# Kernel optimization log

Hardware: AMD Instinct MI355X
Metric: run time of the kernel (lower is better)

Reference implementation:

```python
import jax, jax.numpy as jnp
import numpy as np

N = 96        # num_nodes
D = 64        # emb_size / n_hid
BS = 16
T = 13
G = 1         # num_graph

# all N^2 ordered pairs, receiver-major: edge e=i*N+j has receiver i, sender j
_REC = jnp.repeat(jnp.arange(N), N)
_SEND = jnp.tile(jnp.arange(N), N)


def _lin(shape, key, scale=0.05):
    return (jax.random.normal(key, shape, dtype=jnp.float32) * scale)


def setup_inputs() -> dict:
    key = jax.random.key(0)
    ks = jax.random.split(key, 24)
    inp = {
        "skill_seq": jax.random.randint(ks[0], (BS, T), 0, N, dtype=jnp.int32),
        "adj": jax.random.uniform(ks[1], (G, BS, N, N), dtype=jnp.float32),
        "node_embeddings": jax.random.normal(ks[2], (G, N, D), dtype=jnp.float32),
        # edge MLP
        "W_msg1": _lin((2 * D, D), ks[3]), "b_msg1": jnp.zeros((D,), jnp.float32),
        "W_msg2": _lin((D, D), ks[4]),     "b_msg2": jnp.zeros((D,), jnp.float32),
        # GRU hidden projections (no bias)
        "W_hr": _lin((D, D), ks[5]), "W_hi": _lin((D, D), ks[6]), "W_hh": _lin((D, D), ks[7]),
        # GRU input projections (bias)
        "W_ir": _lin((D, D), ks[8]),  "b_ir": jnp.zeros((D,), jnp.float32),
        "W_ii": _lin((D, D), ks[9]),  "b_ii": jnp.zeros((D,), jnp.float32),
        "W_in": _lin((D, D), ks[10]), "b_in": jnp.zeros((D,), jnp.float32),
        # output MLP
        "W_o1": _lin((D, D), ks[11]), "b_o1": jnp.zeros((D,), jnp.float32),
        "W_o2": _lin((D, D), ks[12]), "b_o2": jnp.zeros((D,), jnp.float32),
        "W_o3": _lin((D, D), ks[13]), "b_o3": jnp.zeros((D,), jnp.float32),
    }
    return inp


def _forward(skill_seq, adj, node_embeddings,
             W_msg1, b_msg1, W_msg2, b_msg2,
             W_hr, W_hi, W_hh,
             W_ir, b_ir, W_ii, b_ii, W_in, b_in,
             W_o1, b_o1, W_o2, b_o2, W_o3, b_o3):
    bs, time_steps = skill_seq.shape
    hidden0 = jnp.zeros((G, bs, N, D), dtype=adj.dtype)
    emb = node_embeddings[0]  # [N, D] (num_graph=1)

    def step(hidden, skill_t):
        # gather senders/receivers over the node axis -> [G, bs, N^2, 2D]
        senders = hidden[:, :, _SEND, :]
        receivers = hidden[:, :, _REC, :]
        pre_msg = jnp.concatenate([senders, receivers], axis=-1)
        msg = jnp.tanh(pre_msg @ W_msg1 + b_msg1)        # [G, bs, N^2, D]
        msg = jnp.tanh(msg @ W_msg2 + b_msg2)
        msg = msg.reshape(G, bs, N, N, D)                # receiver i, sender j
        # mask by adjacency and scatter-sum over senders, then /N
        agg = jnp.einsum('gbij,gbijd->gbid', adj, msg) / N   # [G, bs, N, D]
        inputs = emb[skill_t][None, :, None, :]          # [1, bs, 1, D]
        r = jax.nn.sigmoid(inputs @ W_ir + b_ir + agg @ W_hr)
        i = jax.nn.sigmoid(inputs @ W_ii + b_ii + agg @ W_hi)
        n = jnp.tanh(inputs @ W_in + b_in + r * (agg @ W_hh))
        hidden = (1.0 - i) * n + i * hidden
        pred = jax.nn.relu(hidden @ W_o1 + b_o1)
        pred = jax.nn.relu(pred @ W_o2 + b_o2)
        pred = pred @ W_o3 + b_o3                        # [G, bs, N, D]
        return hidden, pred

    skills_t = skill_seq[:, :time_steps - 1].T           # [T-1, bs]
    _, preds = jax.lax.scan(step, hidden0, skills_t)     # [T-1, G, bs, N, D]
    # torch: stack(dim=1) -> [G, T-1, bs, N, D]; transpose(1,2) -> [G, bs, T-1, N, D]
    return jnp.transpose(preds, (1, 2, 0, 3, 4))


def reference(skill_seq, adj, node_embeddings,
              W_msg1, b_msg1, W_msg2, b_msg2,
              W_hr, W_hi, W_hh,
              W_ir, b_ir, W_ii, b_ii, W_in, b_in,
              W_o1, b_o1, W_o2, b_o2, W_o3, b_o3):
    return _forward(skill_seq, adj, node_embeddings,
                    W_msg1, b_msg1, W_msg2, b_msg2,
                    W_hr, W_hi, W_hh,
                    W_ir, b_ir, W_ii, b_ii, W_in, b_in,
                    W_o1, b_o1, W_o2, b_o2, W_o3, b_o3)
```

## Files before the change

### kernel.cpp

```cpp
#include <hip/hip_runtime.h>

typedef unsigned short ushort_t;
typedef __attribute__((ext_vector_type(8))) short short8;
typedef __attribute__((ext_vector_type(8))) __bf16 bf16x8;
typedef __attribute__((ext_vector_type(4))) float floatx4;

#define NN 96
#define DD 64
#define BSZ 16
#define TSTEP 12
#define JSPLIT 4
#define JPW 24
#define ITILES 6

#define OFF_HALL  0u
#define OFF_E     5111808u
#define OFF_S0    5185536u
#define OFF_S1    5578752u
#define OFF_R0    5971968u
#define OFF_R1    6365184u
#define OFF_PART  6758400u
#define OFF_WSWZ  9904128u
#define OFF_CNT   9977856u
#define HSLOT     98304

union fragU  { short8 s; bf16x8 b; };
union packU  { floatx4 f; unsigned long long u[2]; };

static __device__ __forceinline__ short f2bf(float f){
    union { float f; unsigned u; } v; v.f = f;
    unsigned u = v.u;
    u += 0x7fffu + ((u >> 16) & 1u);
    return (short)(u >> 16);
}
static __device__ __forceinline__ float fast_tanh(float x){
    float p = __expf(2.f * x);
    return (p - 1.f) * __builtin_amdgcn_rcpf(p + 1.f);
}
static __device__ __forceinline__ float fast_sigmoid(float x){
    float p = __expf(-x);
    return __builtin_amdgcn_rcpf(1.f + p);
}
static __device__ __forceinline__ void zero4(floatx4* a){
    floatx4 z = {0.f,0.f,0.f,0.f};
    a[0]=z; a[1]=z; a[2]=z; a[3]=z;
}
static __device__ __forceinline__ floatx4 aload4(const float* p){
    const unsigned long long* s = (const unsigned long long*)p;
    packU pk;
    pk.u[0] = __hip_atomic_load(s,     __ATOMIC_RELAXED, __HIP_MEMORY_SCOPE_AGENT);
    pk.u[1] = __hip_atomic_load(s + 1, __ATOMIC_RELAXED, __HIP_MEMORY_SCOPE_AGENT);
    return pk.f;
}
static __device__ __forceinline__ void astore4(float* p, floatx4 v){
    unsigned long long* d = (unsigned long long*)p;
    packU pk; pk.f = v;
    __hip_atomic_store(d,     pk.u[0], __ATOMIC_RELAXED, __HIP_MEMORY_SCOPE_AGENT);
    __hip_atomic_store(d + 1, pk.u[1], __ATOMIC_RELAXED, __HIP_MEMORY_SCOPE_AGENT);
}
static __device__ __forceinline__ void buildA(const float* sM, int col, int quad, short8& a0, short8& a1){
    floatx4 f0 = *(const floatx4*)&sM[col*68 + quad*8];
    floatx4 f1 = *(const floatx4*)&sM[col*68 + quad*8 + 4];
    floatx4 f2 = *(const floatx4*)&sM[col*68 + 32 + quad*8];
    floatx4 f3 = *(const floatx4*)&sM[col*68 + 32 + quad*8 + 4];
    fragU u0, u1;
    #pragma unroll
    for (int jj = 0; jj < 4; jj++){
        u0.b[jj]   = (__bf16)f0[jj];
        u0.b[4+jj] = (__bf16)f1[jj];
        u1.b[jj]   = (__bf16)f2[jj];
        u1.b[4+jj] = (__bf16)f3[jj];
    }
    a0 = u0.s; a1 = u1.s;
}
static __device__ __forceinline__ void mm16(short8 a0, short8 a1, const short8* wzm, int l, floatx4* acc){
    #pragma unroll
    for (int nt = 0; nt < 4; nt++){
        short8 b0 = wzm[nt*64 + l];
        short8 b1 = wzm[(4 + nt)*64 + l];
        acc[nt] = __builtin_amdgcn_mfma_f32_16x16x32_bf16(a0, b0, acc[nt], 0, 0, 0);
        acc[nt] = __builtin_amdgcn_mfma_f32_16x16x32_bf16(a1, b1, acc[nt], 0, 0, 0);
    }
}
static __device__ __forceinline__ void mm16r(short8 a0, short8 a1, const short8* f, floatx4* acc){
    #pragma unroll
    for (int nt = 0; nt < 4; nt++){
        acc[nt] = __builtin_amdgcn_mfma_f32_16x16x32_bf16(a0, f[nt],     acc[nt], 0, 0, 0);
        acc[nt] = __builtin_amdgcn_mfma_f32_16x16x32_bf16(a1, f[4 + nt], acc[nt], 0, 0, 0);
    }
}

__global__ __launch_bounds__(256) void k_init(
    const float* __restrict__ emb, const float* __restrict__ Wmsg1,
    const float* __restrict__ Wmsg2,
    const float* __restrict__ Whr, const float* __restrict__ Whi, const float* __restrict__ Whh,
    const float* __restrict__ Wir, const float* __restrict__ bir,
    const float* __restrict__ Wii, const float* __restrict__ bii,
    const float* __restrict__ Win, const float* __restrict__ bin,
    const float* __restrict__ Wo1, const float* __restrict__ Wo2, const float* __restrict__ Wo3,
    int* __restrict__ cnt, float* __restrict__ Ef, ushort_t* __restrict__ wswz)
{
    int wg = blockIdx.x, tid = threadIdx.x;
    if (wg < 72) {
        int flat = wg*256 + tid;
        int m = flat / 6144; int r = flat % 6144; int s = r >> 6; int d = r & 63;
        const float* W = (m==0)? Wir : (m==1)? Wii : Win;
        const float* B = (m==0)? bir : (m==1)? bii : bin;
        float acc = B[d];
        #pragma unroll 8
        for (int k = 0; k < 64; k++)
            acc += emb[s*64 + k] * W[k*64 + d];
        Ef[flat] = acc;
        if (wg < 5) {
            int c = wg*256 + tid;
            if (c < TSTEP*BSZ*ITILES) cnt[c] = 0;
        }
    } else {
        int flat = (wg - 72)*256 + tid;
        int m = flat >> 12; int q = flat & 4095;
        int jj = q & 7, lane = (q >> 3) & 63, nt = (q >> 9) & 3, kc = q >> 11;
        int k = kc*32 + ((lane >> 4) << 3) + jj;
        int n = nt*16 + (lane & 15);
        const float* src; int idx = k*64 + n;
        switch (m) {
          case 0: src = Wmsg2; break;
          case 1: src = Whr;  break;
          case 2: src = Whi;  break;
          case 3: src = Whh;  break;
          case 4: src = Wmsg1; break;
          case 5: src = Wmsg1; idx = (64 + k)*64 + n; break;
          case 6: src = Wo1; break;
          case 7: src = Wo2; break;
          default: src = Wo3; break;
        }
        wswz[flat] = (ushort_t)f2bf(src[idx]);
    }
}

__global__ __launch_bounds__(256) void k_step0(
    const float* __restrict__ adj, const float* __restrict__ b1in, const float* __restrict__ b2in,
    const int* __restrict__ skills, const float* __restrict__ Ef,
    const ushort_t* __restrict__ wswz,
    float* __restrict__ hall, float* __restrict__ S1, float* __restrict__ R1)
{
    __shared__ float sM[16*68];
    __shared__ float sG[3][16*68];
    __shared__ float sE[3*64];
    __shared__ float sRS[16*17];
    int wg = blockIdx.x; int b = wg / 6, it = wg % 6;
    int tid = threadIdx.x; int w = tid >> 6; int l = tid & 63;
    int quad = l >> 4, col = l & 15;

    {
        int i = tid >> 4, seg = tid & 15;
        const float* arow = &adj[(b*NN + it*16 + i)*NN + seg*6];
        float s = 0.f;
        #pragma unroll
        for (int j = 0; j < 6; j++) s += arow[j];
        sRS[i*17 + seg] = s;
    }
    if (tid < 192) {
        int s = skills[b*13 + 0];
        sE[tid] = Ef[(tid >> 6)*6144 + s*64 + (tid & 63)];
    }
    __syncthreads();
    if (tid < 16) {
        float s = 0.f;
        #pragma unroll
        for (int q = 0; q < 16; q++) s += sRS[tid*17 + q];
        sRS[tid*17 + 16] = s * (1.f/96.f);
    }
    __syncthreads();

    if (w == 0) {
        float b2v[4];
        #pragma unroll
        for (int nt = 0; nt < 4; nt++) b2v[nt] = b2in[nt*16 + col];
        fragU u0, u1;
        #pragma unroll
        for (int e = 0; e < 8; e++) {
            u0.b[e] = (__bf16)fast_tanh(b1in[quad*8 + e]);
            u1.b[e] = (__bf16)fast_tanh(b1in[32 + quad*8 + e]);
        }
        floatx4 acc[4];
        zero4(acc);
        mm16(u0.s, u1.s, (const short8*)wswz + 0*512, l, acc);
        #pragma unroll
        for (int nt = 0; nt < 4; nt++)
          #pragma unroll
          for (int r = 0; r < 4; r++) {
            float m = fast_tanh(acc[nt][r] + b2v[nt]);
            sM[(quad*4 + r)*68 + nt*16 + col] = sRS[(quad*4 + r)*17 + 16] * m;
          }
    }
    __syncthreads();

    if (w < 3) {
        short8 a0, a1;
        buildA(sM, col, quad, a0, a1);
        floatx4 acc[4];
        zero4(acc);
        mm16(a0, a1, (const short8*)wswz + (1 + w)*512, l, acc);
        #pragma unroll
        for (int nt = 0; nt < 4; nt++)
          #pragma unroll
          for (int r = 0; r < 4; r++)
            sG[w][(quad*4 + r)*68 + nt*16 + col] = acc[nt][r];
    }
    __syncthreads();

    {
        int i = tid >> 4, k4 = (tid & 15)*4;
        float h[4];
        #pragma unroll
        for (int e = 0; e < 4; e++) {
            int d = k4 + e;
            float gi = fast_sigmoid(sE[64 + d] + sG[1][i*68 + d]);
            float gr = fast_sigmoid(sE[d]      + sG[0][i*68 + d]);
            float nv = fast_tanh  (sE[128 + d] + gr * sG[2][i*68 + d]);
            h[e] = (1.f - gi)*nv;
        }
        #pragma unroll
        for (int e = 0; e < 4; e++) sM[i*68 + k4 + e] = h[e];
        floatx4 hv = { h[0], h[1], h[2], h[3] };
        *(floatx4*)&hall[(size_t)1*HSLOT + (b*NN + it*16 + i)*64 + k4] = hv;
    }
    __syncthreads();

    if (w < 2) {
        short8 a0, a1;
        buildA(sM, col, quad, a0, a1);
        floatx4 acc[4];
        zero4(acc);
        mm16(a0, a1, (const short8*)wswz + (4 + w)*512, l, acc);
        float* dst = (w == 0) ? S1 : R1;
        #pragma unroll
        for (int nt = 0; nt < 4; nt++)
          #pragma unroll
          for (int r = 0; r < 4; r++)
            dst[(b*NN + it*16 + quad*4 + r)*64 + nt*16 + col] = acc[nt][r];
    }
}

__global__ __launch_bounds__(512, 2) void k_step(
    const float* __restrict__ adj, const float* __restrict__ b1in, const float* __restrict__ b2in,
    const float* __restrict__ Sread, const float* __restrict__ Rread,
    const ushort_t* __restrict__ wswz, float* __restrict__ partial,
    const int* __restrict__ skills, const float* __restrict__ Ef,
    const float* __restrict__ hprev, float* __restrict__ hcur,
    float* __restrict__ Swrite, float* __restrict__ Rwrite,
    int* __restrict__ cnt, int t)
{
    __shared__ float lds[11712];
    __shared__ int sLast;
    float* sS   = lds;
    float* sRB  = lds + 1536;
    float* sAdj = lds + 2624;
    float* sAgg = lds + 3008;

    int wg = blockIdx.x;
    int js = wg / 96; int rem = wg % 96; int b = rem / 6; int it = rem % 6;
    int tid = threadIdx.x; int w = tid >> 6; int l = tid & 63;
    int quad = l >> 4, col = l & 15;
    int j0 = js * JPW;

    for (int q = tid; q < JPW*16; q += 512) {
        int row = q >> 4, c4 = (q & 15) * 4;
        *(floatx4*)&sS[row*64 + c4] = *(const floatx4*)&Sread[(b*NN + j0 + row)*64 + c4];
    }
    if (tid < 256) {
        int row = tid >> 4, c4 = (tid & 15) * 4;
        floatx4 r4 = *(const floatx4*)&Rread[(b*NN + it*16 + row)*64 + c4];
        floatx4 b4 = *(const floatx4*)&b1in[c4];
        floatx4 o = r4 + b4;
        *(floatx4*)&sRB[row*68 + c4] = o;
    }
    if (tid < 16*JPW) {
        int i = tid / JPW, j = tid % JPW;
        sAdj[tid] = adj[(b*NN + it*16 + i)*NN + j0 + j];
    }
    const short8* wz = (const short8*)wswz;
    short8 w2f[2][4];
    #pragma unroll
    for (int kc = 0; kc < 2; kc++)
      #pragma unroll
      for (int nt = 0; nt < 4; nt++)
        w2f[kc][nt] = wz[(kc*4 + nt)*64 + l];
    float b2v[4];
    #pragma unroll
    for (int nt = 0; nt < 4; nt++) b2v[nt] = b2in[nt*16 + col];
    __syncthreads();

    float rbv[16];
    #pragma unroll
    for (int c = 0; c < 4; c++)
        *(floatx4*)&rbv[c*4] = *(const floatx4*)&sRB[col*68 + (c>>1)*32 + quad*8 + (c&1)*4];

    float agg[4][4];
    #pragma unroll
    for (int nt=0;nt<4;nt++)
      #pragma unroll
      for (int r=0;r<4;r++) agg[nt][r] = 0.f;

    #pragma unroll
    for (int c = 0; c < 3; c++) {
        int jl = w*3 + c;
        float sv[16];
        #pragma unroll
        for (int cc = 0; cc < 4; cc++)
            *(floatx4*)&sv[cc*4] = *(const floatx4*)&sS[jl*64 + (cc>>1)*32 + quad*8 + (cc&1)*4];
        fragU u0, u1;
        #pragma unroll
        for (int e = 0; e < 8; e++) {
            u0.b[e] = (__bf16)fast_tanh(sv[e]   + rbv[e]);
            u1.b[e] = (__bf16)fast_tanh(sv[8+e] + rbv[8+e]);
        }
        floatx4 acc[4];
        zero4(acc);
        #pragma unroll
        for (int nt = 0; nt < 4; nt++) {
            acc[nt] = __builtin_amdgcn_mfma_f32_16x16x32_bf16(u0.s, w2f[0][nt], acc[nt], 0,0,0);
            acc[nt] = __builtin_amdgcn_mfma_f32_16x16x32_bf16(u1.s, w2f[1][nt], acc[nt], 0,0,0);
        }
        float adjv[4];
        #pragma unroll
        for (int r = 0; r < 4; r++) adjv[r] = sAdj[(quad*4 + r)*JPW + jl];
        #pragma unroll
        for (int nt = 0; nt < 4; nt++)
          #pragma unroll
          for (int r = 0; r < 4; r++)
            agg[nt][r] += adjv[r] * fast_tanh(acc[nt][r] + b2v[nt]);
    }
    #pragma unroll
    for (int nt = 0; nt < 4; nt++)
      #pragma unroll
      for (int r = 0; r < 4; r++)
        sAgg[w*1088 + (quad*4 + r)*68 + nt*16 + col] = agg[nt][r];
    __syncthreads();
    if (tid < 256) {
        int i = tid >> 4, k4 = (tid & 15) * 4;
        floatx4 o = {0.f,0.f,0.f,0.f};
        #pragma unroll
        for (int s8 = 0; s8 < 8; s8++)
            o += *(const floatx4*)&sAgg[s8*1088 + i*68 + k4];
        o = o * (1.f/96.f);
        astore4(&partial[((js*BSZ + b)*NN + it*16 + i)*64 + k4], o);
    }
    if (t == TSTEP - 1) return;

    __syncthreads();
    if (tid == 0) {
        int old = atomicAdd(&cnt[t*(BSZ*ITILES) + b*ITILES + it], 1);
        sLast = (old == JSPLIT - 1);
    }
    __syncthreads();
    if (!sLast) return;

    float* sM = lds;
    float* sG = lds + 1088;
    float* sH = lds + 4352;
    float* sE = lds + 5376;

    const short8* wzb = (const short8*)wswz;
    short8 fG[8], fSR[8];
    if (w < 3) {
        #pragma unroll
        for (int q = 0; q < 8; q++) fG[q] = wzb[(1 + w)*512 + q*64 + l];
    }
    if (w < 2) {
        #pragma unroll
        for (int q = 0; q < 8; q++) fSR[q] = wzb[(4 + w)*512 + q*64 + l];
    }

    if (tid < 256) {
        int i = tid >> 4, k4 = (tid & 15) * 4;
        floatx4 a = {0.f,0.f,0.f,0.f};
        #pragma unroll
        for (int p = 0; p < JSPLIT; p++)
            a += aload4(&partial[((p*BSZ + b)*NN + it*16 + i)*64 + k4]);
        *(floatx4*)&sM[i*68 + k4] = a;
        *(floatx4*)&sH[i*64 + k4] = *(const floatx4*)&hprev[(b*NN + it*16 + i)*64 + k4];
    } else if (tid < 448) {
        int q = tid - 256;
        int s = skills[b*13 + t];
        sE[q] = Ef[(q >> 6)*6144 + s*64 + (q & 63)];
    }
    __syncthreads();

    if (w < 3) {
        short8 a0, a1;
        buildA(sM, col, quad, a0, a1);
        floatx4 acc[4];
        zero4(acc);
        mm16r(a0, a1, fG, acc);
        #pragma unroll
        for (int nt = 0; nt < 4; nt++)
          #pragma unroll
          for (int r = 0; r < 4; r++)
            sG[w*1088 + (quad*4 + r)*68 + nt*16 + col] = acc[nt][r];
    }
    __syncthreads();

    if (tid < 256) {
        int i = tid >> 4, k4 = (tid & 15) * 4;
        float h[4];
        #pragma unroll
        for (int e = 0; e < 4; e++) {
            int d = k4 + e;
            float gr = fast_sigmoid(sE[d]       + sG[0*1088 + i*68 + d]);
            float gi = fast_sigmoid(sE[64 + d]  + sG[1*1088 + i*68 + d]);
            float nv = fast_tanh  (sE[128 + d] + gr * sG[2*1088 + i*68 + d]);
            h[e] = (1.f - gi)*nv + gi*sH[i*64 + d];
        }
        #pragma unroll
        for (int e = 0; e < 4; e++) sM[i*68 + k4 + e] = h[e];
        floatx4 hv = { h[0], h[1], h[2], h[3] };
        *(floatx4*)&hcur[(b*NN + it*16 + i)*64 + k4] = hv;
    }
    __syncthreads();

    if (w < 2) {
        short8 a0, a1;
        buildA(sM, col, quad, a0, a1);
        floatx4 acc[4];
        zero4(acc);
        mm16r(a0, a1, fSR, acc);
        float* dst = (w == 0) ? Swrite : Rwrite;
        #pragma unroll
        for (int nt = 0; nt < 4; nt++)
          #pragma unroll
          for (int r = 0; r < 4; r++)
            dst[(b*NN + it*16 + quad*4 + r)*64 + nt*16 + col] = acc[nt][r];
    }
}

__global__ __launch_bounds__(256) void k_out(
    const int* __restrict__ skills, const float* __restrict__ partial,
    const float* __restrict__ Ef, const float* __restrict__ hall,
    const ushort_t* __restrict__ wswz,
    const float* __restrict__ bo1, const float* __restrict__ bo2, const float* __restrict__ bo3,
    float* __restrict__ out)
{
    __shared__ float sT[4][16*68];
    int tid = threadIdx.x; int w = tid >> 6; int l = tid & 63;
    int quad = l >> 4, col = l & 15;
    int g = blockIdx.x*4 + w;
    int ts = g / 96; int rem = g % 96; int b = rem / 6, it = rem % 6;
    float* sm = sT[w];

    if (ts < 11) {
        const float* hsrc = hall + (size_t)(ts + 1)*HSLOT + (b*NN + it*16)*64;
        int i = l >> 2, c0 = (l & 3)*16;
        #pragma unroll
        for (int cc = 0; cc < 4; cc++)
            *(floatx4*)&sm[i*68 + c0 + cc*4] = *(const floatx4*)&hsrc[i*64 + c0 + cc*4];
    } else {
        int i = l >> 2, c0 = (l & 3)*16;
        floatx4 a[4]; zero4(a);
        for (int p = 0; p < JSPLIT; p++) {
            const float* base = &partial[((p*BSZ + b)*NN + it*16 + i)*64 + c0];
            #pragma unroll
            for (int cc = 0; cc < 4; cc++) a[cc] += *(const floatx4*)&base[cc*4];
        }
        #pragma unroll
        for (int cc = 0; cc < 4; cc++) *(floatx4*)&sm[i*68 + c0 + cc*4] = a[cc];

        short8 a0, a1; buildA(sm, col, quad, a0, a1);
        floatx4 Ar[4], Ai[4], Ah[4];
        zero4(Ar); zero4(Ai); zero4(Ah);
        mm16(a0, a1, (const short8*)wswz + 1*512, l, Ar);
        mm16(a0, a1, (const short8*)wswz + 2*512, l, Ai);
        mm16(a0, a1, (const short8*)wswz + 3*512, l, Ah);
        int s = skills[b*13 + 11];
        const float* hp = hall + 11*(size_t)HSLOT;
        #pragma unroll
        for (int nt = 0; nt < 4; nt++) {
            int d = nt*16 + col;
            float er = Ef[0*6144 + s*64 + d];
            float ei = Ef[1*6144 + s*64 + d];
            float en = Ef[2*6144 + s*64 + d];
            #pragma unroll
            for (int r = 0; r < 4; r++) {
                int row = it*16 + quad*4 + r;
                float gr = fast_sigmoid(er + Ar[nt][r]);
                float gi = fast_sigmoid(ei + Ai[nt][r]);
                float nv = fast_tanh  (en + gr*Ah[nt][r]);
                sm[(quad*4 + r)*68 + d] = (1.f - gi)*nv + gi*hp[(b*NN + row)*64 + d];
            }
        }
    }

    float bv1[4], bv2[4], bv3[4];
    #pragma unroll
    for (int nt = 0; nt < 4; nt++) {
        bv1[nt] = bo1[nt*16 + col];
        bv2[nt] = bo2[nt*16 + col];
        bv3[nt] = bo3[nt*16 + col];
    }
    short8 a0, a1;
    floatx4 acc[4];

    buildA(sm, col, quad, a0, a1);
    zero4(acc);
    mm16(a0, a1, (const short8*)wswz + 6*512, l, acc);
    #pragma unroll
    for (int nt = 0; nt < 4; nt++)
      #pragma unroll
      for (int r = 0; r < 4; r++)
        sm[(quad*4 + r)*68 + nt*16 + col] = fmaxf(0.f, acc[nt][r] + bv1[nt]);

    buildA(sm, col, quad, a0, a1);
    zero4(acc);
    mm16(a0, a1, (const short8*)wswz + 7*512, l, acc);
    #pragma unroll
    for (int nt = 0; nt < 4; nt++)
      #pragma unroll
      for (int r = 0; r < 4; r++)
        sm[(quad*4 + r)*68 + nt*16 + col] = fmaxf(0.f, acc[nt][r] + bv2[nt]);

    buildA(sm, col, quad, a0, a1);
    zero4(acc);
    mm16(a0, a1, (const short8*)wswz + 8*512, l, acc);
    #pragma unroll
    for (int nt = 0; nt < 4; nt++)
      #pragma unroll
      for (int r = 0; r < 4; r++)
        out[((b*TSTEP + ts)*NN + it*16 + quad*4 + r)*64 + nt*16 + col] = acc[nt][r] + bv3[nt];
}

extern "C" void kernel_launch(void* const* d_in, const int* in_sizes, int n_in,
                              void* d_out, int out_size, void* d_ws, size_t ws_size,
                              hipStream_t stream) {
    const int*   skills = (const int*)d_in[0];
    const float* adj    = (const float*)d_in[1];
    const float* emb    = (const float*)d_in[2];
    const float* Wmsg1  = (const float*)d_in[3];
    const float* b1     = (const float*)d_in[4];
    const float* Wmsg2  = (const float*)d_in[5];
    const float* b2     = (const float*)d_in[6];
    const float* Whr    = (const float*)d_in[7];
    const float* Whi    = (const float*)d_in[8];
    const float* Whh    = (const float*)d_in[9];
    const float* Wir    = (const float*)d_in[10];
    const float* bir    = (const float*)d_in[11];
    const float* Wii    = (const float*)d_in[12];
    const float* bii    = (const float*)d_in[13];
    const float* Win    = (const float*)d_in[14];
    const float* bin    = (const float*)d_in[15];
    const float* Wo1    = (const float*)d_in[16];
    const float* bo1    = (const float*)d_in[17];
    const float* Wo2    = (const float*)d_in[18];
    const float* bo2    = (const float*)d_in[19];
    const float* Wo3    = (const float*)d_in[20];
    const float* bo3    = (const float*)d_in[21];

    char* ws = (char*)d_ws;
    float*    hall    = (float*)(ws + OFF_HALL);
    float*    Ef      = (float*)(ws + OFF_E);
    float*    S0      = (float*)(ws + OFF_S0);
    float*    S1      = (float*)(ws + OFF_S1);
    float*    R0      = (float*)(ws + OFF_R0);
    float*    R1      = (float*)(ws + OFF_R1);
    float*    partial = (float*)(ws + OFF_PART);
    ushort_t* wswz    = (ushort_t*)(ws + OFF_WSWZ);
    int*      cnt     = (int*)(ws + OFF_CNT);
    float*    out     = (float*)d_out;

    k_init<<<dim3(216), dim3(256), 0, stream>>>(emb, Wmsg1, Wmsg2, Whr, Whi, Whh,
        Wir, bir, Wii, bii, Win, bin, Wo1, Wo2, Wo3, cnt, Ef, wswz);

    k_step0<<<dim3(BSZ*ITILES), dim3(256), 0, stream>>>(
        adj, b1, b2, skills, Ef, wswz, hall, S1, R1);

    for (int t = 1; t < TSTEP; t++) {
        const float* Sr = (t & 1) ? S1 : S0;
        const float* Rr = (t & 1) ? R1 : R0;
        float*       Sw = (t & 1) ? S0 : S1;
        float*       Rw = (t & 1) ? R0 : R1;
        k_step<<<dim3(JSPLIT*BSZ*ITILES), dim3(512), 0, stream>>>(
            adj, b1, b2, Sr, Rr, wswz, partial, skills, Ef,
            hall + (size_t)t*HSLOT, hall + (size_t)(t+1)*HSLOT,
            Sw, Rw, cnt, t);
    }
    k_out<<<dim3(288), dim3(256), 0, stream>>>(skills, partial, Ef, hall, wswz,
        bo1, bo2, bo3, out);
}
```

Measured before the change: 253.2 us.

## Fold step0 into init kernel and reuse own partial in last-block reduction

```diff
diff --git a/kernel.cpp b/kernel.cpp
--- a/kernel.cpp
+++ b/kernel.cpp
@@ -89,6 +89,23 @@
         acc[nt] = __builtin_amdgcn_mfma_f32_16x16x32_bf16(a1, f[4 + nt], acc[nt], 0, 0, 0);
     }
 }
+static __device__ __forceinline__ short8 fragB(const float* W, int l, int kc, int nt, int koff){
+    short8 r;
+    int kbase = koff + kc*32 + ((l >> 4) << 3);
+    int n = nt*16 + (l & 15);
+    #pragma unroll
+    for (int jj = 0; jj < 8; jj++) r[jj] = f2bf(W[(kbase + jj)*64 + n]);
+    return r;
+}
+static __device__ __forceinline__ void mm16g(short8 a0, short8 a1, const float* W, int koff, int l, floatx4* acc){
+    #pragma unroll
+    for (int nt = 0; nt < 4; nt++){
+        short8 b0 = fragB(W, l, 0, nt, koff);
+        short8 b1 = fragB(W, l, 1, nt, koff);
+        acc[nt] = __builtin_amdgcn_mfma_f32_16x16x32_bf16(a0, b0, acc[nt], 0, 0, 0);
+        acc[nt] = __builtin_amdgcn_mfma_f32_16x16x32_bf16(a1, b1, acc[nt], 0, 0, 0);
+    }
+}
 
 __global__ __launch_bounds__(256) void k_init(
     const float* __restrict__ emb, const float* __restrict__ Wmsg1,
@@ -98,8 +115,16 @@
     const float* __restrict__ Wii, const float* __restrict__ bii,
     const float* __restrict__ Win, const float* __restrict__ bin,
     const float* __restrict__ Wo1, const float* __restrict__ Wo2, const float* __restrict__ Wo3,
-    int* __restrict__ cnt, float* __restrict__ Ef, ushort_t* __restrict__ wswz)
+    const float* __restrict__ adj, const float* __restrict__ b1in, const float* __restrict__ b2in,
+    const int* __restrict__ skills,
+    int* __restrict__ cnt, float* __restrict__ Ef, ushort_t* __restrict__ wswz,
+    float* __restrict__ hall, float* __restrict__ S1, float* __restrict__ R1)
 {
+    __shared__ float sM[16*68];
+    __shared__ float sG[3][16*68];
+    __shared__ float sE[3*64];
+    __shared__ float sRS[16*17];
+
     int wg = blockIdx.x, tid = threadIdx.x;
     if (wg < 72) {
         int flat = wg*256 + tid;
@@ -115,7 +140,9 @@
             int c = wg*256 + tid;
             if (c < TSTEP*BSZ*ITILES) cnt[c] = 0;
         }
-    } else {
+        return;
+    }
+    if (wg < 216) {
         int flat = (wg - 72)*256 + tid;
         int m = flat >> 12; int q = flat & 4095;
         int jj = q & 7, lane = (q >> 3) & 63, nt = (q >> 9) & 3, kc = q >> 11;
@@ -134,21 +161,11 @@
           default: src = Wo3; break;
         }
         wswz[flat] = (ushort_t)f2bf(src[idx]);
-    }
-}
-
-__global__ __launch_bounds__(256) void k_step0(
-    const float* __restrict__ adj, const float* __restrict__ b1in, const float* __restrict__ b2in,
-    const int* __restrict__ skills, const float* __restrict__ Ef,
-    const ushort_t* __restrict__ wswz,
-    float* __restrict__ hall, float* __restrict__ S1, float* __restrict__ R1)
-{
-    __shared__ float sM[16*68];
-    __shared__ float sG[3][16*68];
-    __shared__ float sE[3*64];
-    __shared__ float sRS[16*17];
-    int wg = blockIdx.x; int b = wg / 6, it = wg % 6;
-    int tid = threadIdx.x; int w = tid >> 6; int l = tid & 63;
+        return;
+    }
+
+    int tile = wg - 216; int b = tile / 6, it = tile % 6;
+    int w = tid >> 6; int l = tid & 63;
     int quad = l >> 4, col = l & 15;
 
     {
@@ -160,8 +177,15 @@
         sRS[i*17 + seg] = s;
     }
     if (tid < 192) {
+        int m = tid >> 6, d = tid & 63;
         int s = skills[b*13 + 0];
-        sE[tid] = Ef[(tid >> 6)*6144 + s*64 + (tid & 63)];
+        const float* W = (m==0)? Wir : (m==1)? Wii : Win;
+        const float* B = (m==0)? bir : (m==1)? bii : bin;
+        float acc = B[d];
+        #pragma unroll 8
+        for (int k = 0; k < 64; k++)
+            acc += emb[s*64 + k] * W[k*64 + d];
+        sE[tid] = acc;
     }
     __syncthreads();
     if (tid < 16) {
@@ -184,7 +208,7 @@
         }
         floatx4 acc[4];
         zero4(acc);
-        mm16(u0.s, u1.s, (const short8*)wswz + 0*512, l, acc);
+        mm16g(u0.s, u1.s, Wmsg2, 0, l, acc);
         #pragma unroll
         for (int nt = 0; nt < 4; nt++)
           #pragma unroll
@@ -196,11 +220,12 @@
     __syncthreads();
 
     if (w < 3) {
+        const float* Wg = (w==0)? Whr : (w==1)? Whi : Whh;
         short8 a0, a1;
         buildA(sM, col, quad, a0, a1);
         floatx4 acc[4];
         zero4(acc);
-        mm16(a0, a1, (const short8*)wswz + (1 + w)*512, l, acc);
+        mm16g(a0, a1, Wg, 0, l, acc);
         #pragma unroll
         for (int nt = 0; nt < 4; nt++)
           #pragma unroll
@@ -232,7 +257,7 @@
         buildA(sM, col, quad, a0, a1);
         floatx4 acc[4];
         zero4(acc);
-        mm16(a0, a1, (const short8*)wswz + (4 + w)*512, l, acc);
+        mm16g(a0, a1, Wmsg1, w*64, l, acc);
         float* dst = (w == 0) ? S1 : R1;
         #pragma unroll
         for (int nt = 0; nt < 4; nt++)
@@ -263,6 +288,7 @@
     int tid = threadIdx.x; int w = tid >> 6; int l = tid & 63;
     int quad = l >> 4, col = l & 15;
     int j0 = js * JPW;
+    floatx4 myp;
 
     for (int q = tid; q < JPW*16; q += 512) {
         int row = q >> 4, c4 = (q & 15) * 4;
@@ -344,7 +370,10 @@
         for (int s8 = 0; s8 < 8; s8++)
             o += *(const floatx4*)&sAgg[s8*1088 + i*68 + k4];
         o = o * (1.f/96.f);
-        astore4(&partial[((js*BSZ + b)*NN + it*16 + i)*64 + k4], o);
+        myp = o;
+        float* dstp = &partial[((js*BSZ + b)*NN + it*16 + i)*64 + k4];
+        if (t == TSTEP - 1) *(floatx4*)dstp = o;
+        else                astore4(dstp, o);
     }
     if (t == TSTEP - 1) return;
 
@@ -376,8 +405,10 @@
         int i = tid >> 4, k4 = (tid & 15) * 4;
         floatx4 a = {0.f,0.f,0.f,0.f};
         #pragma unroll
-        for (int p = 0; p < JSPLIT; p++)
-            a += aload4(&partial[((p*BSZ + b)*NN + it*16 + i)*64 + k4]);
+        for (int p = 0; p < JSPLIT; p++) {
+            if (p == js) a += myp;
+            else         a += aload4(&partial[((p*BSZ + b)*NN + it*16 + i)*64 + k4]);
+        }
         *(floatx4*)&sM[i*68 + k4] = a;
         *(floatx4*)&sH[i*64 + k4] = *(const floatx4*)&hprev[(b*NN + it*16 + i)*64 + k4];
     } else if (tid < 448) {
@@ -566,11 +597,9 @@
     int*      cnt     = (int*)(ws + OFF_CNT);
     float*    out     = (float*)d_out;
 
-    k_init<<<dim3(216), dim3(256), 0, stream>>>(emb, Wmsg1, Wmsg2, Whr, Whi, Whh,
-        Wir, bir, Wii, bii, Win, bin, Wo1, Wo2, Wo3, cnt, Ef, wswz);
-
-    k_step0<<<dim3(BSZ*ITILES), dim3(256), 0, stream>>>(
-        adj, b1, b2, skills, Ef, wswz, hall, S1, R1);
+    k_init<<<dim3(312), dim3(256), 0, stream>>>(emb, Wmsg1, Wmsg2, Whr, Whi, Whh,
+        Wir, bir, Wii, bii, Win, bin, Wo1, Wo2, Wo3,
+        adj, b1, b2, skills, cnt, Ef, wswz, hall, S1, R1);
 
     for (int t = 1; t < TSTEP; t++) {
         const float* Sr = (t & 1) ? S1 : S0;
```

Measured after the change: 253.6 us. No clear change (+0.1%).
